# Kernel optimization log

Hardware: AMD Instinct MI355X
Metric: run time of the kernel (lower is better)

Reference implementation:

```python
import jax, jax.numpy as jnp
import numpy as np

R = 64  # all tensor-ring ranks equal

def setup_inputs() -> dict:
    key = jax.random.key(0)
    k1, k2, k3 = jax.random.split(key, 3)
    B, T, N, M, C = 512, 64, 512, 64, 100
    # xavier-uniform-ish scale for weights (gain=init_value=1.0)
    s_sh = float(np.sqrt(6.0 / (R * N + R)))
    s_la = float(np.sqrt(6.0 / (C * R * M + R)))
    return {
        "tensor": jax.random.normal(k1, (B, T, N), dtype=jnp.float32),
        "W_shared": jax.random.uniform(k2, (R, N, R), dtype=jnp.float32, minval=-s_sh, maxval=s_sh),
        "W_last": jax.random.uniform(k3, (C, R, M, R), dtype=jnp.float32, minval=-s_la, maxval=s_la),
    }

def reference(tensor, W_shared, W_last):
    B = tensor.shape[0]
    xt = jnp.transpose(tensor, (1, 0, 2))  # [T, B, N]
    state0 = jnp.ones((R, B, R), dtype=tensor.dtype)  # [r1, B, r2]
    # per-step: x = einsum('bj,rbi->rbji'); state = einsum('ijk,rbji->rbk')
    # == einsum('bj,rbi,ijk->rbk'); factored to avoid the [r,b,n,r] intermediate
    def step(state, x_t):
        bik = jnp.einsum('bj,ijk->bik', x_t, W_shared)   # [B, r2, r3]
        new = jnp.einsum('rbi,bik->rbk', state, bik)     # [r1, B, r3]
        return new, None
    state, _ = jax.lax.scan(step, state0, xt)
    # last kernel with pad_input = ones(B, m):
    # einsum('cijk,rbji->cbrk') with x[r,b,j,i]=state[r,b,i] == sum over j of W_last
    W_sum = jnp.sum(W_last, axis=2)                      # [C, r2, r_last]
    state = jnp.einsum('cik,rbi->cbrk', W_sum, state)    # [C, B, r1, r_last]
    # trace over the last two (square) rank dims
    out = jnp.einsum('cbrr->cb', state)                  # [C, B]
    return out
```

## Files before the change

kernel.cpp:

```cpp
#include <hip/hip_runtime.h>
#include <hip/hip_fp16.h>


typedef _Float16 f16;
typedef __attribute__((ext_vector_type(8))) _Float16 f16x8;
typedef __attribute__((ext_vector_type(2))) _Float16 f16x2;
typedef __attribute__((ext_vector_type(4))) float f32x4;

#define GLDS16(g, l)                                                      \
    __builtin_amdgcn_global_load_lds(                                     \
        (const __attribute__((address_space(1))) void*)(g),               \
        (__attribute__((address_space(3))) void*)(l), 16, 0, 0)

#define BARRIER() asm volatile("s_barrier" ::: "memory")
#define VMCNT(n) asm volatile("s_waitcnt vmcnt(" #n ")" ::: "memory")

__global__ __launch_bounds__(256) void k_usum(const float* __restrict__ Wl,
                                              float* __restrict__ u) {
    int ci = blockIdx.x;
    const float4* p = (const float4*)(Wl + (size_t)ci * 4096);
    int tid = threadIdx.x;
    float s = 0.f;
#pragma unroll
    for (int q = 0; q < 4; ++q) {
        float4 v = p[tid + 256 * q];
        s += v.x + v.y + v.z + v.w;
    }
    __shared__ float red[256];
    red[tid] = s;
    __syncthreads();
    if (tid < 128) red[tid] += red[tid + 128];
    __syncthreads();
    if (tid < 64) {
        float x = red[tid] + red[tid + 64];
#pragma unroll
        for (int off = 32; off > 0; off >>= 1) x += __shfl_down(x, off, 64);
        if (tid == 0) u[ci] = x;
    }
}

__global__ __launch_bounds__(256) void k_cvtA(const float* __restrict__ in,
                                              f16* __restrict__ out) {
    int idx = blockIdx.x * 256 + threadIdx.x;
    const float4* p = (const float4*)in + (size_t)idx * 2;
    float4 v0 = p[0], v1 = p[1];
    f16x8 h;
    h[0] = (f16)v0.x; h[1] = (f16)v0.y; h[2] = (f16)v0.z; h[3] = (f16)v0.w;
    h[4] = (f16)v1.x; h[5] = (f16)v1.y; h[6] = (f16)v1.z; h[7] = (f16)v1.w;
    *(f16x8*)(out + (size_t)idx * 8) = h;
}

__global__ __launch_bounds__(256) void k_cvtW(const float* __restrict__ W,
                                              f16* __restrict__ Bt) {
    int o = blockIdx.x * 256 + threadIdx.x;
    int col = o >> 8;
    int j = (o & 255) << 1;
    int i = col >> 6, k = col & 63;
    const float* src = W + ((size_t)i * 512 + j) * 64 + k;
    f16x2 pk;
    pk[0] = (f16)src[0];
    pk[1] = (f16)src[64];
    *(f16x2*)(Bt + (size_t)col * 512 + j) = pk;
}


#define STAGE_A(qq, ha, ktv) do {                                             \
    _Pragma("unroll") for (int u_ = 0; u_ < 2; ++u_) {                        \
        int idx_ = (wid * 2 + u_) * 64 + lane;                                \
        int r_ = idx_ >> 3;                                                   \
        int ls_ = (idx_ & 7) ^ (r_ & 7);                                      \
        const f16* g_ = A + (size_t)(m0 + (ha) * 128 + r_) * 512              \
                          + (ktv) * 64 + ls_ * 8;                             \
        char* l_ = smem + (qq) * 65536 + (ha) * 16384 + (wid * 2 + u_) * 1024;\
        GLDS16(g_, l_);                                                       \
    } } while (0)

#define STAGE_B(qq, hb, ktv) do {                                             \
    _Pragma("unroll") for (int u_ = 0; u_ < 2; ++u_) {                        \
        int idx_ = (wid * 2 + u_) * 64 + lane;                                \
        int r_ = idx_ >> 3;                                                   \
        int ls_ = (idx_ & 7) ^ (r_ & 7);                                      \
        const f16* g_ = Bt + (size_t)(n0 + (hb) * 128 + r_) * 512             \
                           + (ktv) * 64 + ls_ * 8;                            \
        char* l_ = smem + (qq) * 65536 + 32768 + (hb) * 16384                 \
                        + (wid * 2 + u_) * 1024;                              \
        GLDS16(g_, l_);                                                       \
    } } while (0)

#define RD_A(ha, ktv) do {                                                    \
    _Pragma("unroll") for (int mf_ = 0; mf_ < 4; ++mf_)                       \
    _Pragma("unroll") for (int kq_ = 0; kq_ < 2; ++kq_) {                     \
        int ra_ = wr * 64 + mf_ * 16 + (lane & 15);                           \
        int off_ = ((ra_ << 7) + kq_ * 64 + ((lane >> 4) << 4))               \
                   ^ ((ra_ & 7) << 4);                                        \
        a[mf_][kq_] = *(const f16x8*)(smem + ((ktv) & 1) * 65536              \
                                      + (ha) * 16384 + off_);                 \
    } } while (0)

#define RD_B(hb, ktv, breg) do {                                              \
    _Pragma("unroll") for (int nf_ = 0; nf_ < 2; ++nf_)                       \
    _Pragma("unroll") for (int kq_ = 0; kq_ < 2; ++kq_) {                     \
        int rb_ = wc * 32 + nf_ * 16 + (lane & 15);                           \
        int off_ = ((rb_ << 7) + kq_ * 64 + ((lane >> 4) << 4))               \
                   ^ ((rb_ & 7) << 4);                                        \
        breg[nf_][kq_] = *(const f16x8*)(smem + ((ktv) & 1) * 65536           \
                                         + 32768 + (hb) * 16384 + off_);      \
    } } while (0)

#define MFMA_Q(qa_, qb_, breg) do {                                           \
    __builtin_amdgcn_s_setprio(1);                                            \
    _Pragma("unroll") for (int mf_ = 0; mf_ < 4; ++mf_)                       \
    _Pragma("unroll") for (int nf_ = 0; nf_ < 2; ++nf_)                       \
    _Pragma("unroll") for (int kq_ = 0; kq_ < 2; ++kq_)                       \
        acc[qa_][qb_][mf_][nf_] = __builtin_amdgcn_mfma_f32_16x16x32_f16(     \
            a[mf_][kq_], breg[nf_][kq_], acc[qa_][qb_][mf_][nf_], 0, 0, 0);   \
    __builtin_amdgcn_s_setprio(0);                                            \
    } while (0)

__global__ __launch_bounds__(512) void k_gemm_256(const f16* __restrict__ A,
                                                  const f16* __restrict__ Bt,
                                                  __half* __restrict__ outp) {
    extern __shared__ char smem[];
    const int tid = threadIdx.x;
    const int lane = tid & 63;
    const int wid = tid >> 6;
    int lin = blockIdx.x;
    int swz = (lin & 7) * 256 + (lin >> 3);
    const int n0 = (swz & 15) * 256;
    const int m0 = (swz >> 4) * 256;
    const int wr = wid >> 2, wc = wid & 3;

    f32x4 acc[2][2][4][2];
#pragma unroll
    for (int x = 0; x < 2; ++x)
#pragma unroll
        for (int y = 0; y < 2; ++y)
#pragma unroll
            for (int z = 0; z < 4; ++z)
#pragma unroll
                for (int w = 0; w < 2; ++w) acc[x][y][z][w] = (f32x4)0.f;

    f16x8 a[4][2], b0[2][2], b1[2][2];

    STAGE_A(0, 0, 0);
    STAGE_B(0, 0, 0);
    STAGE_B(0, 1, 0);
    STAGE_A(0, 1, 0);
    STAGE_A(1, 0, 1);
    STAGE_B(1, 0, 1);
    STAGE_B(1, 1, 1);
    VMCNT(10);
    BARRIER();

    for (int kt = 0; kt < 6; ++kt) {
        RD_A(0, kt);
        RD_B(0, kt, b0);
        STAGE_A((kt + 1) & 1, 1, kt + 1);
        VMCNT(10);
        BARRIER();
        MFMA_Q(0, 0, b0);
        BARRIER();
        RD_B(1, kt, b1);
        STAGE_A(kt & 1, 0, kt + 2);
        VMCNT(10);
        BARRIER();
        MFMA_Q(0, 1, b1);
        BARRIER();
        RD_A(1, kt);
        STAGE_B(kt & 1, 0, kt + 2);
        BARRIER();
        MFMA_Q(1, 0, b0);
        BARRIER();
        STAGE_B(kt & 1, 1, kt + 2);
        VMCNT(10);
        BARRIER();
        MFMA_Q(1, 1, b1);
        BARRIER();
    }
    {
        RD_A(0, 6);
        RD_B(0, 6, b0);
        STAGE_A(1, 1, 7);
        VMCNT(10);
        BARRIER();
        MFMA_Q(0, 0, b0);
        BARRIER();
        RD_B(1, 6, b1);
        VMCNT(8);
        BARRIER();
        MFMA_Q(0, 1, b1);
        BARRIER();
        RD_A(1, 6);
        BARRIER();
        MFMA_Q(1, 0, b0);
        BARRIER();
        VMCNT(4);
        BARRIER();
        MFMA_Q(1, 1, b1);
        BARRIER();
    }
    {
        RD_A(0, 7);
        RD_B(0, 7, b0);
        VMCNT(2);
        BARRIER();
        MFMA_Q(0, 0, b0);
        BARRIER();
        RD_B(1, 7, b1);
        VMCNT(0);
        BARRIER();
        MFMA_Q(0, 1, b1);
        BARRIER();
        RD_A(1, 7);
        BARRIER();
        MFMA_Q(1, 0, b0);
        BARRIER();
        BARRIER();
        MFMA_Q(1, 1, b1);
        BARRIER();
    }

    __half* Cs = (__half*)smem;
#pragma unroll
    for (int qa = 0; qa < 2; ++qa)
#pragma unroll
        for (int qb = 0; qb < 2; ++qb)
#pragma unroll
            for (int mf = 0; mf < 4; ++mf)
#pragma unroll
                for (int nf = 0; nf < 2; ++nf)
#pragma unroll
                    for (int j = 0; j < 4; ++j) {
                        int row = qa * 128 + wr * 64 + mf * 16 + ((lane >> 4) << 2) + j;
                        int col = qb * 128 + wc * 32 + nf * 16 + (lane & 15);
                        Cs[row * 256 + col] = __float2half(acc[qa][qb][mf][nf][j]);
                    }
    BARRIER();
#pragma unroll
    for (int it = 0; it < 16; ++it) {
        int idx = it * 512 + tid;
        int r = idx >> 5, seg = idx & 31;
        *(float4*)(outp + (size_t)(m0 + r) * 4096 + n0 + seg * 8) =
            *(const float4*)(Cs + r * 256 + seg * 8);
    }
}

#define BM 128
#define BN 64
#define BK 32
__global__ __launch_bounds__(256) void k_gemm(const float* __restrict__ A,
                                              const float* __restrict__ W,
                                              __half* __restrict__ out,
                                              int a_off, int a_stride) {
    __shared__ float As[BK * BM];
    __shared__ float Bs[BK * BN];
    int i0 = blockIdx.x;
    int m0 = blockIdx.y * BM;
    int tid = threadIdx.x;
    int tx = tid & 15, ty = tid >> 4;
    float acc[8][4];
#pragma unroll
    for (int q = 0; q < 8; ++q)
#pragma unroll
        for (int c = 0; c < 4; ++c) acc[q][c] = 0.f;
    const float* wbase = W + (size_t)i0 * 32768;
    for (int j0 = 0; j0 < 512; j0 += BK) {
        {
            int c4 = tid & 7;
            int r = tid >> 3;
#pragma unroll
            for (int p = 0; p < 4; ++p) {
                int row = r + 32 * p;
                float4 v = *(const float4*)(A + (size_t)a_off +
                                            (size_t)(m0 + row) * a_stride + j0 + 4 * c4);
                As[(4 * c4 + 0) * BM + row] = v.x;
                As[(4 * c4 + 1) * BM + row] = v.y;
                As[(4 * c4 + 2) * BM + row] = v.z;
                As[(4 * c4 + 3) * BM + row] = v.w;
            }
            const float4* src = (const float4*)(wbase + (size_t)j0 * 64);
            float4* dst = (float4*)Bs;
            dst[tid] = src[tid];
            dst[tid + 256] = src[tid + 256];
        }
        __syncthreads();
#pragma unroll
        for (int kk = 0; kk < BK; ++kk) {
            float bv[4], av[8];
#pragma unroll
            for (int c = 0; c < 4; ++c) bv[c] = Bs[kk * BN + 4 * tx + c];
#pragma unroll
            for (int q = 0; q < 8; ++q) av[q] = As[kk * BM + 8 * ty + q];
#pragma unroll
            for (int q = 0; q < 8; ++q)
#pragma unroll
                for (int c = 0; c < 4; ++c) acc[q][c] += av[q] * bv[c];
        }
        __syncthreads();
    }
#pragma unroll
    for (int q = 0; q < 8; ++q) {
        int m = m0 + 8 * ty + q;
        __half* o = out + (size_t)m * 4096 + i0 * 64 + 4 * tx;
#pragma unroll
        for (int c = 0; c < 4; ++c) o[c] = __float2half(acc[q][c]);
    }
}

__global__ __launch_bounds__(256) void k_scan(const __half* __restrict__ bik,
                                              float* __restrict__ v_all) {
    int b = blockIdx.x;
    int tid = threadIdx.x;
    int k = tid & 63, grp = tid >> 6;
    __shared__ float vsh[64];
    __shared__ float part[256];
    if (tid < 64) vsh[tid] = 1.0f;
    const __half* base = bik + (size_t)b * 64 * 4096 + grp * 16 * 64 + k;
    __half bufA[16], bufB[16];
#pragma unroll
    for (int q = 0; q < 16; ++q) bufA[q] = base[q * 64];
    __syncthreads();
    for (int t = 0; t < 64; t += 2) {
        {
            const __half* pn = base + (size_t)(t + 1) * 4096;
#pragma unroll
            for (int q = 0; q < 16; ++q) bufB[q] = pn[q * 64];
            float s = 0.f;
#pragma unroll
            for (int q = 0; q < 16; ++q) s += vsh[grp * 16 + q] * __half2float(bufA[q]);
            part[tid] = s;
            __syncthreads();
            if (tid < 64) vsh[k] = part[k] + part[64 + k] + part[128 + k] + part[192 + k];
            __syncthreads();
        }
        {
            int t2 = (t + 2 < 64) ? (t + 2) : 63;
            const __half* pn = base + (size_t)t2 * 4096;
#pragma unroll
            for (int q = 0; q < 16; ++q) bufA[q] = pn[q * 64];
            float s = 0.f;
#pragma unroll
            for (int q = 0; q < 16; ++q) s += vsh[grp * 16 + q] * __half2float(bufB[q]);
            part[tid] = s;
            __syncthreads();
            if (tid < 64) vsh[k] = part[k] + part[64 + k] + part[128 + k] + part[192 + k];
            __syncthreads();
        }
    }
    if (tid < 64) v_all[(size_t)b * 64 + tid] = vsh[tid];
}

__global__ __launch_bounds__(256) void k_update(const __half* __restrict__ Mt,
                                                const float* __restrict__ vin,
                                                float* __restrict__ vout, int first) {
    int o = blockIdx.x * 256 + threadIdx.x;
    int b = o >> 6, k = o & 63;
    const __half* m = Mt + (size_t)b * 4096;
    float s = 0.f;
    if (first) {
#pragma unroll 8
        for (int i = 0; i < 64; ++i) s += __half2float(m[i * 64 + k]);
    } else {
        const float* v = vin + (size_t)b * 64;
#pragma unroll 8
        for (int i = 0; i < 64; ++i) s += v[i] * __half2float(m[i * 64 + k]);
    }
    vout[o] = s;
}

__global__ __launch_bounds__(256) void k_final(const float* __restrict__ u,
                                               const float* __restrict__ v,
                                               float* __restrict__ out) {
    int o = blockIdx.x * 256 + threadIdx.x;
    int c = o >> 9, b = o & 511;
    const float* uc = u + c * 64;
    const float* vb = v + (size_t)b * 64;
    float s = 0.f;
#pragma unroll 8
    for (int i = 0; i < 64; ++i) s += uc[i] * vb[i];
    out[o] = s;
}

extern "C" void kernel_launch(void* const* d_in, const int* in_sizes, int n_in,
                              void* d_out, int out_size, void* d_ws, size_t ws_size,
                              hipStream_t stream) {
    const float* tensor = (const float*)d_in[0];
    const float* Wsh = (const float*)d_in[1];
    const float* Wl = (const float*)d_in[2];
    float* out = (float*)d_out;
    char* ws = (char*)d_ws;

    const size_t bik_bytes = (size_t)32768 * 4096 * sizeof(__half);
    const size_t fast_bytes = bik_bytes + (512u << 10) + ((size_t)16777216 * 2) + ((size_t)4096 * 512 * 2);

    if (ws_size >= fast_bytes) {
        __half* bik = (__half*)ws;
        float* u = (float*)(ws + bik_bytes);
        float* v = (float*)(ws + bik_bytes + (256u << 10));
        f16* Af16 = (f16*)(ws + bik_bytes + (512u << 10));
        f16* Btw = Af16 + (size_t)16777216;

        k_cvtA<<<8192, 256, 0, stream>>>(tensor, Af16);
        k_cvtW<<<4096, 256, 0, stream>>>(Wsh, Btw);
        k_usum<<<6400, 256, 0, stream>>>(Wl, u);
        (void)hipFuncSetAttribute((const void*)k_gemm_256,
                                  hipFuncAttributeMaxDynamicSharedMemorySize, 131072);
        k_gemm_256<<<2048, 512, 131072, stream>>>(Af16, Btw, bik);
        k_scan<<<512, 256, 0, stream>>>(bik, v);
        k_final<<<200, 256, 0, stream>>>(u, v, out);
    } else if (ws_size >= bik_bytes + (2u << 20)) {
        __half* bik = (__half*)ws;
        float* u = (float*)(ws + bik_bytes);
        float* v = (float*)(ws + bik_bytes + (64 << 10));

        k_usum<<<6400, 256, 0, stream>>>(Wl, u);
        dim3 g(64, 256);
        k_gemm<<<g, 256, 0, stream>>>(tensor, Wsh, bik, 0, 512);
        k_scan<<<512, 256, 0, stream>>>(bik, v);
        k_final<<<200, 256, 0, stream>>>(u, v, out);
    } else {
        __half* bikt = (__half*)ws;
        float* u = (float*)(ws + (size_t)(4 << 20));
        float* v0 = (float*)(ws + (size_t)(4 << 20) + (64 << 10));
        float* v1 = v0 + 32768;

        k_usum<<<6400, 256, 0, stream>>>(Wl, u);
        for (int t = 0; t < 64; ++t) {
            dim3 g(64, 4);
            k_gemm<<<g, 256, 0, stream>>>(tensor, Wsh, bikt, t * 512, 32768);
            float* vin = (t & 1) ? v0 : v1;
            float* vout = (t & 1) ? v1 : v0;
            k_update<<<128, 256, 0, stream>>>(bikt, (t == 0) ? v0 : vin, vout, t == 0);
        }
        k_final<<<200, 256, 0, stream>>>(u, v1, out);
    }
}
```

Measured before the change: 288.2 us.

## Restructure GEMM pipeline waits/barriers and fuse final contraction into scan

Reorders the k_gemm_256 main loop so each k-tile has a single vmcnt wait plus barrier at its top. Most intermediate waits and barriers are removed, and LDS reads, staging and MFMAs interleave more freely. Separately, the final trace contraction (u·v per class) moves into the tail of k_scan, which drops the k_final launch and the v round trip through memory. The main risk is that fewer barriers could open LDS read/write races between stages that reuse buffers.

```diff
diff --git a/kernel.cpp b/kernel.cpp
--- a/kernel.cpp
+++ b/kernel.cpp
@@ -149,72 +149,56 @@
     STAGE_A(1, 0, 1);
     STAGE_B(1, 0, 1);
     STAGE_B(1, 1, 1);
-    VMCNT(10);
-    BARRIER();
 
     for (int kt = 0; kt < 6; ++kt) {
+        VMCNT(6);
+        BARRIER();
         RD_A(0, kt);
         RD_B(0, kt, b0);
         STAGE_A((kt + 1) & 1, 1, kt + 1);
-        VMCNT(10);
-        BARRIER();
         MFMA_Q(0, 0, b0);
         BARRIER();
         RD_B(1, kt, b1);
+        MFMA_Q(0, 1, b1);
+        BARRIER();
+        RD_A(1, kt);
         STAGE_A(kt & 1, 0, kt + 2);
-        VMCNT(10);
-        BARRIER();
-        MFMA_Q(0, 1, b1);
-        BARRIER();
-        RD_A(1, kt);
         STAGE_B(kt & 1, 0, kt + 2);
-        BARRIER();
         MFMA_Q(1, 0, b0);
         BARRIER();
         STAGE_B(kt & 1, 1, kt + 2);
-        VMCNT(10);
-        BARRIER();
         MFMA_Q(1, 1, b1);
         BARRIER();
     }
     {
+        VMCNT(6);
+        BARRIER();
         RD_A(0, 6);
         RD_B(0, 6, b0);
         STAGE_A(1, 1, 7);
-        VMCNT(10);
-        BARRIER();
         MFMA_Q(0, 0, b0);
         BARRIER();
         RD_B(1, 6, b1);
-        VMCNT(8);
-        BARRIER();
         MFMA_Q(0, 1, b1);
         BARRIER();
         RD_A(1, 6);
-        BARRIER();
         MFMA_Q(1, 0, b0);
         BARRIER();
-        VMCNT(4);
-        BARRIER();
         MFMA_Q(1, 1, b1);
         BARRIER();
     }
     {
+        VMCNT(0);
+        BARRIER();
         RD_A(0, 7);
         RD_B(0, 7, b0);
-        VMCNT(2);
-        BARRIER();
         MFMA_Q(0, 0, b0);
         BARRIER();
         RD_B(1, 7, b1);
-        VMCNT(0);
-        BARRIER();
         MFMA_Q(0, 1, b1);
         BARRIER();
         RD_A(1, 7);
-        BARRIER();
         MFMA_Q(1, 0, b0);
-        BARRIER();
         BARRIER();
         MFMA_Q(1, 1, b1);
         BARRIER();
@@ -308,7 +292,8 @@
 }
 
 __global__ __launch_bounds__(256) void k_scan(const __half* __restrict__ bik,
-                                              float* __restrict__ v_all) {
+                                              const float* __restrict__ u,
+                                              float* __restrict__ out) {
     int b = blockIdx.x;
     int tid = threadIdx.x;
     int k = tid & 63, grp = tid >> 6;
@@ -347,7 +332,13 @@
             __syncthreads();
         }
     }
-    if (tid < 64) v_all[(size_t)b * 64 + tid] = vsh[tid];
+    if (tid < 100) {
+        const float* uc = u + tid * 64;
+        float s = 0.f;
+#pragma unroll 8
+        for (int i = 0; i < 64; ++i) s += uc[i] * vsh[i];
+        out[tid * 512 + b] = s;
+    }
 }
 
 __global__ __launch_bounds__(256) void k_update(const __half* __restrict__ Mt,
@@ -396,7 +387,6 @@
     if (ws_size >= fast_bytes) {
         __half* bik = (__half*)ws;
         float* u = (float*)(ws + bik_bytes);
-        float* v = (float*)(ws + bik_bytes + (256u << 10));
         f16* Af16 = (f16*)(ws + bik_bytes + (512u << 10));
         f16* Btw = Af16 + (size_t)16777216;
 
@@ -406,18 +396,15 @@
         (void)hipFuncSetAttribute((const void*)k_gemm_256,
                                   hipFuncAttributeMaxDynamicSharedMemorySize, 131072);
         k_gemm_256<<<2048, 512, 131072, stream>>>(Af16, Btw, bik);
-        k_scan<<<512, 256, 0, stream>>>(bik, v);
-        k_final<<<200, 256, 0, stream>>>(u, v, out);
+        k_scan<<<512, 256, 0, stream>>>(bik, u, out);
     } else if (ws_size >= bik_bytes + (2u << 20)) {
         __half* bik = (__half*)ws;
         float* u = (float*)(ws + bik_bytes);
-        float* v = (float*)(ws + bik_bytes + (64 << 10));
 
         k_usum<<<6400, 256, 0, stream>>>(Wl, u);
         dim3 g(64, 256);
         k_gemm<<<g, 256, 0, stream>>>(tensor, Wsh, bik, 0, 512);
-        k_scan<<<512, 256, 0, stream>>>(bik, v);
-        k_final<<<200, 256, 0, stream>>>(u, v, out);
+        k_scan<<<512, 256, 0, stream>>>(bik, u, out);
     } else {
         __half* bikt = (__half*)ws;
         float* u = (float*)(ws + (size_t)(4 << 20));
```

Measured after the change: 282.8 us. No clear change (-1.9%).
